# Kernel optimization log

Measured on AMD Instinct MI355X. Metric: run time of the kernel, lower is better.

Reference implementation:

```python
import jax, jax.numpy as jnp
import numpy as np

HIDDEN = 1024
HEADS = 16
HEAD_DIM = HIDDEN // HEADS  # 64
B, S = 2, 2048


def setup_inputs() -> dict:
    key = jax.random.key(0)
    ks = jax.random.split(key, 8)
    scale = 1.0 / np.sqrt(HIDDEN)
    return {
        "hidden_states": jax.random.normal(ks[0], (B, S, HIDDEN), dtype=jnp.float32),
        "head_mask": jnp.ones((1, HEADS, 1, 1), dtype=jnp.float32),
        "Wq": jax.random.normal(ks[1], (HIDDEN, HIDDEN), dtype=jnp.float32) * scale,
        "bq": jnp.zeros((HIDDEN,), dtype=jnp.float32),
        "Wk": jax.random.normal(ks[2], (HIDDEN, HIDDEN), dtype=jnp.float32) * scale,
        "bk": jnp.zeros((HIDDEN,), dtype=jnp.float32),
        "Wv": jax.random.normal(ks[3], (HIDDEN, HIDDEN), dtype=jnp.float32) * scale,
        "bv": jnp.zeros((HIDDEN,), dtype=jnp.float32),
    }


def _split_heads(x):
    # [B, S, HIDDEN] -> [B, HEADS, S, HEAD_DIM]
    b, s, _ = x.shape
    return x.reshape(b, s, HEADS, HEAD_DIM).transpose(0, 2, 1, 3)


def reference(hidden_states, head_mask, Wq, bq, Wk, bk, Wv, bv):
    q = _split_heads(hidden_states @ Wq + bq)
    k = _split_heads(hidden_states @ Wk + bk)
    v = _split_heads(hidden_states @ Wv + bv)
    # [B, H, S, S] attention scores (eager, full matrix as in original)
    scores = jnp.einsum("bhqd,bhkd->bhqk", q, k) / jnp.sqrt(jnp.float32(HEAD_DIM))
    probs = jax.nn.softmax(scores, axis=-1)
    probs = probs * head_mask  # post-softmax multiplicative head mask
    ctx = jnp.einsum("bhqk,bhkd->bhqd", probs, v)
    b, h, s, d = ctx.shape
    return ctx.transpose(0, 2, 1, 3).reshape(b, s, h * d)
```

## Files before the change

kernel.cpp:

```cpp
#include <hip/hip_runtime.h>
#include <hip/hip_bf16.h>
#include <stdint.h>

#define B_  2
#define S_  2048
#define H_  16
#define D_  64
#define HID 1024

typedef __bf16 bf16x8 __attribute__((ext_vector_type(8)));
typedef float  f32x4  __attribute__((ext_vector_type(4)));
typedef float  f32x16 __attribute__((ext_vector_type(16)));
typedef unsigned int u32x4 __attribute__((ext_vector_type(4)));
typedef unsigned short ush;

__device__ __forceinline__ ush f2bf(float f) {
    __bf16 b = (__bf16)f;
    return __builtin_bit_cast(ush, b);
}
__device__ __forceinline__ unsigned pk2(float a, float b) {
    return (unsigned)f2bf(a) | ((unsigned)f2bf(b) << 16);
}
__device__ __forceinline__ float xchg32f(float x) {
    return __shfl_xor(x, 32, 64);
}
__device__ __forceinline__ float exp2fast(float x) {
#if __has_builtin(__builtin_amdgcn_exp2f)
    return __builtin_amdgcn_exp2f(x);
#else
    float r; asm("v_exp_f32 %0, %1" : "=v"(r) : "v"(x)); return r;
#endif
}
__device__ __forceinline__ void gld16(const void* g, void* l) {
    __builtin_amdgcn_global_load_lds(
        (const __attribute__((address_space(1))) unsigned*)g,
        (__attribute__((address_space(3))) unsigned*)l, 16, 0, 0);
}
#define MFMA32(a, b, c) __builtin_amdgcn_mfma_f32_32x32x16_bf16(a, b, c, 0, 0, 0)

__global__ __launch_bounds__(256) void cvt_hid(const float* __restrict__ in,
                                               ush* __restrict__ outp) {
    size_t base = ((size_t)blockIdx.x * 256 + threadIdx.x) * 16;
    #pragma unroll
    for (int half = 0; half < 2; ++half) {
        float4 v0 = *reinterpret_cast<const float4*>(in + base + half * 8);
        float4 v1 = *reinterpret_cast<const float4*>(in + base + half * 8 + 4);
        u32x4 o = { pk2(v0.x, v0.y), pk2(v0.z, v0.w),
                    pk2(v1.x, v1.y), pk2(v1.z, v1.w) };
        *reinterpret_cast<u32x4*>(outp + base + half * 8) = o;
    }
}

__global__ __launch_bounds__(256) void wtrans(
    const float* __restrict__ Wq, const float* __restrict__ Wk,
    const float* __restrict__ Wv, ush* __restrict__ wt)
{
    const int tid = threadIdx.x;
    const int k0 = blockIdx.x * 64, n0 = blockIdx.y * 64, sel = blockIdx.z;
    const float* W = sel == 0 ? Wq : (sel == 1 ? Wk : Wv);
    ush* o = wt + (size_t)sel * HID * HID;
    __shared__ ush lT[64][72];
    #pragma unroll
    for (int i = 0; i < 4; ++i) {
        int c = tid + i * 256;
        int kr = c >> 4, c4 = (c & 15) << 2;
        float4 v = *reinterpret_cast<const float4*>(W + (size_t)(k0 + kr) * HID + n0 + c4);
        lT[kr][c4 + 0] = f2bf(v.x); lT[kr][c4 + 1] = f2bf(v.y);
        lT[kr][c4 + 2] = f2bf(v.z); lT[kr][c4 + 3] = f2bf(v.w);
    }
    __syncthreads();
    #pragma unroll
    for (int i = 0; i < 2; ++i) {
        int c = tid + i * 256;
        int nr = c >> 3, k8 = (c & 7) << 3;
        ush t[8];
        #pragma unroll
        for (int u = 0; u < 8; ++u) t[u] = lT[k8 + u][nr];
        u32x4 ov = { (unsigned)t[0] | ((unsigned)t[1] << 16),
                     (unsigned)t[2] | ((unsigned)t[3] << 16),
                     (unsigned)t[4] | ((unsigned)t[5] << 16),
                     (unsigned)t[6] | ((unsigned)t[7] << 16) };
        *reinterpret_cast<u32x4*>(o + (size_t)(n0 + nr) * HID + k0 + k8) = ov;
    }
}

__global__ __launch_bounds__(256) void proj(
    const ush* __restrict__ hidb, const ush* __restrict__ wt,
    const float* __restrict__ bq, const float* __restrict__ bk,
    const float* __restrict__ bv,
    ush* __restrict__ qd, ush* __restrict__ kd, ush* __restrict__ vtd)
{
    const int tid = threadIdx.x;
    const int wave = tid >> 6, lane = tid & 63;
    const int fr = lane & 15, fq = lane >> 4;
    const int wr = wave >> 1, wc = wave & 1;
    const int m0 = blockIdx.x * 128;
    const int n0 = blockIdx.y * 128;
    const int wsel = n0 >> 10;

    __shared__ char pool[65536];

    const int cr = lane >> 3;
    const int cs = lane & 7;

    f32x4 acc[4][4] = {};

    const ush* Asrc = hidb + (size_t)m0 * HID;
    const ush* Bsrc = wt + (size_t)n0 * HID;

    auto stage = [&](int buf, int kk) {
        #pragma unroll
        for (int j = 0; j < 4; ++j) {
            int ch = wave * 4 + j;
            int r = ch * 8 + cr;
            int so = kk + ((cs ^ (r & 7)) << 3);
            gld16(Asrc + (size_t)r * HID + so, pool + buf * 16384 + ch * 1024);
            gld16(Bsrc + (size_t)r * HID + so, pool + 32768 + buf * 16384 + ch * 1024);
        }
    };

    stage(0, 0);
    __syncthreads();
    int buf = 0;
    for (int ks = 0; ks < 16; ++ks) {
        if (ks < 15) stage(buf ^ 1, (ks + 1) * 64);
        const char* ab = pool + buf * 16384;
        const char* bb = pool + 32768 + buf * 16384;
        #pragma unroll
        for (int c = 0; c < 2; ++c) {
            bf16x8 a[4], b[4];
            #pragma unroll
            for (int i = 0; i < 4; ++i) {
                int ra = wr * 64 + i * 16 + fr;
                a[i] = *reinterpret_cast<const bf16x8*>(
                    ab + ((ra * 128 + c * 64 + fq * 16) ^ ((ra & 7) << 4)));
                int rb = wc * 64 + i * 16 + fr;
                b[i] = *reinterpret_cast<const bf16x8*>(
                    bb + ((rb * 128 + c * 64 + fq * 16) ^ ((rb & 7) << 4)));
            }
            __builtin_amdgcn_s_setprio(1);
            #pragma unroll
            for (int i = 0; i < 4; ++i)
                #pragma unroll
                for (int j = 0; j < 4; ++j)
                    acc[i][j] = __builtin_amdgcn_mfma_f32_16x16x32_bf16(
                        a[i], b[j], acc[i][j], 0, 0, 0);
            __builtin_amdgcn_s_setprio(0);
        }
        __syncthreads();
        buf ^= 1;
    }

    const int bi = m0 >> 11;
    const int s0 = m0 & 2047;
    const float* bias = wsel == 0 ? bq : (wsel == 1 ? bk : bv);
    const int nb = n0 & 1023;

    if (wsel < 2) {
        ush* dst = wsel == 0 ? qd : kd;
        const float scale = wsel == 0 ? 0.18033688011112042f : 1.0f;
        #pragma unroll
        for (int j = 0; j < 4; ++j) {
            int n = nb + wc * 64 + j * 16 + fr;
            int hh = n >> 6, d = n & 63;
            float bb2 = bias[n];
            const size_t rowb = (size_t)(bi * H_ + hh) * S_;
            #pragma unroll
            for (int i = 0; i < 4; ++i)
                #pragma unroll
                for (int e = 0; e < 4; ++e) {
                    int s = s0 + wr * 64 + i * 16 + fq * 4 + e;
                    dst[(rowb + s) * D_ + d] = f2bf((acc[i][j][e] + bb2) * scale);
                }
        }
    } else {
        ush (*lT)[136] = (ush (*)[136])pool;
        #pragma unroll
        for (int j = 0; j < 4; ++j) {
            int nl = wc * 64 + j * 16 + fr;
            float bb2 = bias[nb + nl];
            #pragma unroll
            for (int i = 0; i < 4; ++i)
                #pragma unroll
                for (int e = 0; e < 4; ++e)
                    lT[wr * 64 + i * 16 + fq * 4 + e][nl] = f2bf(acc[i][j][e] + bb2);
        }
        __syncthreads();
        #pragma unroll
        for (int c2 = 0; c2 < 8; ++c2) {
            int cid = tid + c2 * 256;
            int nl = cid >> 4, s8 = (cid & 15) * 8;
            int n = nb + nl, hh = n >> 6, d = n & 63;
            ush t[8];
            #pragma unroll
            for (int u = 0; u < 8; ++u) t[u] = lT[s8 + u][nl];
            u32x4 ov = { (unsigned)t[0] | ((unsigned)t[1] << 16),
                         (unsigned)t[2] | ((unsigned)t[3] << 16),
                         (unsigned)t[4] | ((unsigned)t[5] << 16),
                         (unsigned)t[6] | ((unsigned)t[7] << 16) };
            *reinterpret_cast<u32x4*>(
                vtd + ((size_t)(bi * H_ + hh) * D_ + d) * S_ + s0 + s8) = ov;
        }
    }
}

#define STAGE(sb, kv0) do {                                                    \
    gld16(K + (size_t)((kv0) + kr) * D_ + ss,      pool + (sb) * 16384 + wave * 1024); \
    gld16(K + (size_t)((kv0) + 64 + kr) * D_ + ss, pool + (sb) * 16384 + 8192 + wave * 1024); \
    gld16(VT + (size_t)dr * S_ + (kv0) + ss,       pool + 32768 + (sb) * 16384 + wave * 1024); \
    gld16(VT + (size_t)dr * S_ + (kv0) + 64 + ss,  pool + 32768 + (sb) * 16384 + 8192 + wave * 1024); \
} while (0)

#define WAITV0() asm volatile("s_waitcnt vmcnt(0)" ::: "memory")
#define BARRIER() do { __builtin_amdgcn_s_barrier();                           \
                       __builtin_amdgcn_sched_barrier(0); } while (0)

#define EXPC(cA, cB, pA, pB, hb) do {                                          \
    float a0_ = exp2fast(pA[(hb)+0]), a1_ = exp2fast(pA[(hb)+1]);              \
    float a2_ = exp2fast(pA[(hb)+2]), a3_ = exp2fast(pA[(hb)+3]);              \
    float a4_ = exp2fast(pA[(hb)+4]), a5_ = exp2fast(pA[(hb)+5]);              \
    float a6_ = exp2fast(pA[(hb)+6]), a7_ = exp2fast(pA[(hb)+7]);              \
    sA += ((a0_+a1_)+(a2_+a3_)) + ((a4_+a5_)+(a6_+a7_));                       \
    cA = u32x4{pk2(a0_,a1_), pk2(a2_,a3_), pk2(a4_,a5_), pk2(a6_,a7_)};        \
    float b0_ = exp2fast(pB[(hb)+0]), b1_ = exp2fast(pB[(hb)+1]);              \
    float b2_ = exp2fast(pB[(hb)+2]), b3_ = exp2fast(pB[(hb)+3]);              \
    float b4_ = exp2fast(pB[(hb)+4]), b5_ = exp2fast(pB[(hb)+5]);              \
    float b6_ = exp2fast(pB[(hb)+6]), b7_ = exp2fast(pB[(hb)+7]);              \
    sB += ((b0_+b1_)+(b2_+b3_)) + ((b4_+b5_)+(b6_+b7_));                       \
    cB = u32x4{pk2(b0_,b1_), pk2(b2_,b3_), pk2(b4_,b5_), pk2(b6_,b7_)};        \
} while (0)

#define PVC(ksc, cA, cB) do {                                                  \
    const int o_ = l31 * 128 + (ksc) * 32 + hi * 16;                           \
    bf16x8 v0_ = *(const bf16x8*)(vb + (o_ ^ swz));                            \
    bf16x8 v1_ = *(const bf16x8*)(vb + ((o_ + 4096) ^ swz));                   \
    bf16x8 fA_ = __builtin_bit_cast(bf16x8, cA);                               \
    bf16x8 fB_ = __builtin_bit_cast(bf16x8, cB);                               \
    __builtin_amdgcn_s_setprio(1);                                             \
    aA0 = MFMA32(v0_, fA_, aA0); aA1 = MFMA32(v1_, fA_, aA1);                  \
    aB0 = MFMA32(v0_, fB_, aB0); aB1 = MFMA32(v1_, fB_, aB1);                  \
    __builtin_amdgcn_s_setprio(0);                                             \
} while (0)

__global__ __launch_bounds__(512) void attn(
    const ush* __restrict__ qg, const ush* __restrict__ kg,
    const ush* __restrict__ vtg, const float* __restrict__ hm,
    float* __restrict__ out)
{
    const int tid = threadIdx.x;
    const int wave = tid >> 6, lane = tid & 63;
    const int l31 = lane & 31, hi = lane >> 5;
    const int swz = (l31 & 7) << 4;
    const int g = blockIdx.x & 31, qt = blockIdx.x >> 5;
    const int h = g >> 1, bi = g & 1;
    const int qsub = wave & 3, par = wave >> 2;
    const size_t ho = (size_t)(bi * H_ + h) * S_ * D_;
    const ush* Q  = qg + ho;
    const ush* K  = kg + ho;
    const ush* VT = vtg + ho;

    __shared__ __align__(16) char pool[67584];

    const int dr = wave * 8 + (lane >> 3);
    const int kr = (dr & ~12) | ((dr & 4) << 1) | ((dr & 8) >> 1);
    const int ss = ((lane & 7) ^ (lane >> 3)) * 8;

    const int q0 = qt * 256 + qsub * 64 + l31;
    bf16x8 qfA[4], qfB[4];
    #pragma unroll
    for (int ks = 0; ks < 4; ++ks) {
        qfA[ks] = *reinterpret_cast<const bf16x8*>(Q + (size_t)q0 * D_ + ks * 16 + hi * 8);
        qfB[ks] = *reinterpret_cast<const bf16x8*>(Q + (size_t)(q0 + 32) * D_ + ks * 16 + hi * 8);
    }

    f32x16 aA0 = {}, aA1 = {}, aB0 = {}, aB1 = {};
    float sA = 0.f, sB = 0.f;

    STAGE(0, 0);
    WAITV0(); BARRIER();

    for (int s = 0; s < 16; ++s) {
        if (s < 15) STAGE((s + 1) & 1, (s + 1) * 128);
        const char* kb = pool + (s & 1) * 16384 + par * 8192;
        const char* vb = pool + 32768 + (s & 1) * 16384 + par * 8192;

        f32x16 p0A = {}, p1A = {}, p0B = {}, p1B = {};
        #pragma unroll
        for (int ks = 0; ks < 4; ++ks) {
            const int o = l31 * 128 + ks * 32 + hi * 16;
            bf16x8 k0 = *reinterpret_cast<const bf16x8*>(kb + (o ^ swz));
            bf16x8 k1 = *reinterpret_cast<const bf16x8*>(kb + ((o + 4096) ^ swz));
            __builtin_amdgcn_s_setprio(1);
            p0A = MFMA32(k0, qfA[ks], p0A);
            p1A = MFMA32(k1, qfA[ks], p1A);
            p0B = MFMA32(k0, qfB[ks], p0B);
            p1B = MFMA32(k1, qfB[ks], p1B);
            __builtin_amdgcn_s_setprio(0);
        }

        {
            u32x4 cA0, cB0, cA1, cB1, cA2, cB2, cA3, cB3;
            EXPC(cA0, cB0, p0A, p0B, 0);
            PVC(0, cA0, cB0);
            EXPC(cA1, cB1, p0A, p0B, 8);
            PVC(1, cA1, cB1);
            EXPC(cA2, cB2, p1A, p1B, 0);
            PVC(2, cA2, cB2);
            EXPC(cA3, cB3, p1A, p1B, 8);
            PVC(3, cA3, cB3);
        }

        WAITV0(); BARRIER();
    }

    sA += xchg32f(sA);
    sB += xchg32f(sB);
    float* cbase = (float*)pool;
    float* lbase = (float*)(pool + 65536);

    if (par == 1) {
        #pragma unroll
        for (int c = 0; c < 4; ++c) {
            *(f32x4*)(cbase + qsub * 4096 + (0 * 4 + c) * 256 + lane * 4) =
                f32x4{aA0[c * 4], aA0[c * 4 + 1], aA0[c * 4 + 2], aA0[c * 4 + 3]};
            *(f32x4*)(cbase + qsub * 4096 + (1 * 4 + c) * 256 + lane * 4) =
                f32x4{aA1[c * 4], aA1[c * 4 + 1], aA1[c * 4 + 2], aA1[c * 4 + 3]};
            *(f32x4*)(cbase + qsub * 4096 + (2 * 4 + c) * 256 + lane * 4) =
                f32x4{aB0[c * 4], aB0[c * 4 + 1], aB0[c * 4 + 2], aB0[c * 4 + 3]};
            *(f32x4*)(cbase + qsub * 4096 + (3 * 4 + c) * 256 + lane * 4) =
                f32x4{aB1[c * 4], aB1[c * 4 + 1], aB1[c * 4 + 2], aB1[c * 4 + 3]};
        }
        lbase[qsub * 128 + lane * 2]     = sA;
        lbase[qsub * 128 + lane * 2 + 1] = sB;
    }
    __syncthreads();
    if (par == 0) {
        #pragma unroll
        for (int c = 0; c < 4; ++c) {
            f32x4 t;
            t = *(const f32x4*)(cbase + qsub * 4096 + (0 * 4 + c) * 256 + lane * 4);
            aA0[c*4] += t[0]; aA0[c*4+1] += t[1]; aA0[c*4+2] += t[2]; aA0[c*4+3] += t[3];
            t = *(const f32x4*)(cbase + qsub * 4096 + (1 * 4 + c) * 256 + lane * 4);
            aA1[c*4] += t[0]; aA1[c*4+1] += t[1]; aA1[c*4+2] += t[2]; aA1[c*4+3] += t[3];
            t = *(const f32x4*)(cbase + qsub * 4096 + (2 * 4 + c) * 256 + lane * 4);
            aB0[c*4] += t[0]; aB0[c*4+1] += t[1]; aB0[c*4+2] += t[2]; aB0[c*4+3] += t[3];
            t = *(const f32x4*)(cbase + qsub * 4096 + (3 * 4 + c) * 256 + lane * 4);
            aB1[c*4] += t[0]; aB1[c*4+1] += t[1]; aB1[c*4+2] += t[2]; aB1[c*4+3] += t[3];
        }
        const float liA = sA + lbase[qsub * 128 + lane * 2];
        const float liB = sB + lbase[qsub * 128 + lane * 2 + 1];
        const float hmv = hm[h];
        const float invA = hmv / liA, invB = hmv / liB;
        float* orA = out + ((size_t)bi * S_ + q0) * HID + h * D_;
        float* orB = out + ((size_t)bi * S_ + q0 + 32) * HID + h * D_;
        #pragma unroll
        for (int gg = 0; gg < 4; ++gg) {
            f32x4 o0, o1, o2, o3;
            #pragma unroll
            for (int e = 0; e < 4; ++e) {
                o0[e] = aA0[gg * 4 + e] * invA;
                o1[e] = aA1[gg * 4 + e] * invA;
                o2[e] = aB0[gg * 4 + e] * invB;
                o3[e] = aB1[gg * 4 + e] * invB;
            }
            *reinterpret_cast<f32x4*>(orA + gg * 8 + hi * 4)      = o0;
            *reinterpret_cast<f32x4*>(orA + 32 + gg * 8 + hi * 4) = o1;
            *reinterpret_cast<f32x4*>(orB + gg * 8 + hi * 4)      = o2;
            *reinterpret_cast<f32x4*>(orB + 32 + gg * 8 + hi * 4) = o3;
        }
    }
}

extern "C" void kernel_launch(void* const* d_in, const int* in_sizes, int n_in,
                              void* d_out, int out_size, void* d_ws, size_t ws_size,
                              hipStream_t stream) {
    const float* hid = (const float*)d_in[0];
    const float* hm  = (const float*)d_in[1];
    const float* Wq  = (const float*)d_in[2];
    const float* bq  = (const float*)d_in[3];
    const float* Wk  = (const float*)d_in[4];
    const float* bk  = (const float*)d_in[5];
    const float* Wv  = (const float*)d_in[6];
    const float* bv  = (const float*)d_in[7];
    float* out = (float*)d_out;

    const size_t NE = (size_t)B_ * H_ * S_ * D_;
    ush* qws  = (ush*)d_ws;
    ush* kws  = qws + NE;
    ush* vt   = kws + NE;
    ush* hidb = (ush*)d_out;
    ush* wt   = hidb + NE;

    cvt_hid<<<1024, 256, 0, stream>>>(hid, hidb);
    wtrans<<<dim3(16, 16, 3), 256, 0, stream>>>(Wq, Wk, Wv, wt);
    proj<<<dim3(32, 24), 256, 0, stream>>>(hidb, wt, bq, bk, bv, qws, kws, vt);
    attn<<<256, 512, 0, stream>>>(qws, kws, vt, hm, out);
}
```

Baseline: 89.29 us.

## Load K and V fragments directly from global into registers, dropping LDS staging

```diff
diff --git a/kernel.cpp b/kernel.cpp
--- a/kernel.cpp
+++ b/kernel.cpp
@@ -204,17 +204,6 @@
     }
 }
 
-#define STAGE(sb, kv0) do {                                                    \
-    gld16(K + (size_t)((kv0) + kr) * D_ + ss,      pool + (sb) * 16384 + wave * 1024); \
-    gld16(K + (size_t)((kv0) + 64 + kr) * D_ + ss, pool + (sb) * 16384 + 8192 + wave * 1024); \
-    gld16(VT + (size_t)dr * S_ + (kv0) + ss,       pool + 32768 + (sb) * 16384 + wave * 1024); \
-    gld16(VT + (size_t)dr * S_ + (kv0) + 64 + ss,  pool + 32768 + (sb) * 16384 + 8192 + wave * 1024); \
-} while (0)
-
-#define WAITV0() asm volatile("s_waitcnt vmcnt(0)" ::: "memory")
-#define BARRIER() do { __builtin_amdgcn_s_barrier();                           \
-                       __builtin_amdgcn_sched_barrier(0); } while (0)
-
 #define EXPC(cA, cB, pA, pB, hb) do {                                          \
     float a0_ = exp2fast(pA[(hb)+0]), a1_ = exp2fast(pA[(hb)+1]);              \
     float a2_ = exp2fast(pA[(hb)+2]), a3_ = exp2fast(pA[(hb)+3]);              \
@@ -231,14 +220,11 @@
 } while (0)
 
 #define PVC(ksc, cA, cB) do {                                                  \
-    const int o_ = l31 * 128 + (ksc) * 32 + hi * 16;                           \
-    bf16x8 v0_ = *(const bf16x8*)(vb + (o_ ^ swz));                            \
-    bf16x8 v1_ = *(const bf16x8*)(vb + ((o_ + 4096) ^ swz));                   \
     bf16x8 fA_ = __builtin_bit_cast(bf16x8, cA);                               \
     bf16x8 fB_ = __builtin_bit_cast(bf16x8, cB);                               \
     __builtin_amdgcn_s_setprio(1);                                             \
-    aA0 = MFMA32(v0_, fA_, aA0); aA1 = MFMA32(v1_, fA_, aA1);                  \
-    aB0 = MFMA32(v0_, fB_, aB0); aB1 = MFMA32(v1_, fB_, aB1);                  \
+    aA0 = MFMA32(vfA[ksc], fA_, aA0); aA1 = MFMA32(vfB[ksc], fA_, aA1);        \
+    aB0 = MFMA32(vfA[ksc], fB_, aB0); aB1 = MFMA32(vfB[ksc], fB_, aB1);        \
     __builtin_amdgcn_s_setprio(0);                                             \
 } while (0)
 
@@ -250,7 +236,6 @@
     const int tid = threadIdx.x;
     const int wave = tid >> 6, lane = tid & 63;
     const int l31 = lane & 31, hi = lane >> 5;
-    const int swz = (l31 & 7) << 4;
     const int g = blockIdx.x & 31, qt = blockIdx.x >> 5;
     const int h = g >> 1, bi = g & 1;
     const int qsub = wave & 3, par = wave >> 2;
@@ -261,9 +246,7 @@
 
     __shared__ __align__(16) char pool[67584];
 
-    const int dr = wave * 8 + (lane >> 3);
-    const int kr = (dr & ~12) | ((dr & 4) << 1) | ((dr & 8) >> 1);
-    const int ss = ((lane & 7) ^ (lane >> 3)) * 8;
+    const int krow = (l31 & ~12) | ((l31 & 4) << 1) | ((l31 & 8) >> 1);
 
     const int q0 = qt * 256 + qsub * 64 + l31;
     bf16x8 qfA[4], qfB[4];
@@ -276,26 +259,40 @@
     f32x16 aA0 = {}, aA1 = {}, aB0 = {}, aB1 = {};
     float sA = 0.f, sB = 0.f;
 
-    STAGE(0, 0);
-    WAITV0(); BARRIER();
+    bf16x8 kfA[4], kfB[4], vfA[4], vfB[4];
+
+    int kvw = par * 64;
+    {
+        const ush* kb0 = K + (size_t)(kvw + krow) * D_ + hi * 8;
+        const ush* vb0 = VT + (size_t)l31 * S_ + kvw + hi * 8;
+        #pragma unroll
+        for (int ks = 0; ks < 4; ++ks) {
+            kfA[ks] = *(const bf16x8*)(kb0 + ks * 16);
+            kfB[ks] = *(const bf16x8*)(kb0 + 32 * D_ + ks * 16);
+            vfA[ks] = *(const bf16x8*)(vb0 + ks * 16);
+            vfB[ks] = *(const bf16x8*)(vb0 + 32 * S_ + ks * 16);
+        }
+    }
 
     for (int s = 0; s < 16; ++s) {
-        if (s < 15) STAGE((s + 1) & 1, (s + 1) * 128);
-        const char* kb = pool + (s & 1) * 16384 + par * 8192;
-        const char* vb = pool + 32768 + (s & 1) * 16384 + par * 8192;
-
         f32x16 p0A = {}, p1A = {}, p0B = {}, p1B = {};
+        __builtin_amdgcn_s_setprio(1);
         #pragma unroll
         for (int ks = 0; ks < 4; ++ks) {
-            const int o = l31 * 128 + ks * 32 + hi * 16;
-            bf16x8 k0 = *reinterpret_cast<const bf16x8*>(kb + (o ^ swz));
-            bf16x8 k1 = *reinterpret_cast<const bf16x8*>(kb + ((o + 4096) ^ swz));
-            __builtin_amdgcn_s_setprio(1);
-            p0A = MFMA32(k0, qfA[ks], p0A);
-            p1A = MFMA32(k1, qfA[ks], p1A);
-            p0B = MFMA32(k0, qfB[ks], p0B);
-            p1B = MFMA32(k1, qfB[ks], p1B);
-            __builtin_amdgcn_s_setprio(0);
+            p0A = MFMA32(kfA[ks], qfA[ks], p0A);
+            p1A = MFMA32(kfB[ks], qfA[ks], p1A);
+            p0B = MFMA32(kfA[ks], qfB[ks], p0B);
+            p1B = MFMA32(kfB[ks], qfB[ks], p1B);
+        }
+        __builtin_amdgcn_s_setprio(0);
+
+        if (s < 15) {
+            const ush* kb0 = K + (size_t)(kvw + 128 + krow) * D_ + hi * 8;
+            #pragma unroll
+            for (int ks = 0; ks < 4; ++ks) {
+                kfA[ks] = *(const bf16x8*)(kb0 + ks * 16);
+                kfB[ks] = *(const bf16x8*)(kb0 + 32 * D_ + ks * 16);
+            }
         }
 
         {
@@ -310,7 +307,15 @@
             PVC(3, cA3, cB3);
         }
 
-        WAITV0(); BARRIER();
+        if (s < 15) {
+            const ush* vb0 = VT + (size_t)l31 * S_ + kvw + 128 + hi * 8;
+            #pragma unroll
+            for (int ks = 0; ks < 4; ++ks) {
+                vfA[ks] = *(const bf16x8*)(vb0 + ks * 16);
+                vfB[ks] = *(const bf16x8*)(vb0 + 32 * S_ + ks * 16);
+            }
+        }
+        kvw += 128;
     }
 
     sA += xchg32f(sA);
```

New measurement: 111.3 us. 24.7% more time.

## Split attention KV range four ways per block and double grid size

Applied to the files above, without the earlier changes.

```diff
diff --git a/kernel.cpp b/kernel.cpp
--- a/kernel.cpp
+++ b/kernel.cpp
@@ -205,10 +205,12 @@
 }
 
 #define STAGE(sb, kv0) do {                                                    \
-    gld16(K + (size_t)((kv0) + kr) * D_ + ss,      pool + (sb) * 16384 + wave * 1024); \
-    gld16(K + (size_t)((kv0) + 64 + kr) * D_ + ss, pool + (sb) * 16384 + 8192 + wave * 1024); \
-    gld16(VT + (size_t)dr * S_ + (kv0) + ss,       pool + 32768 + (sb) * 16384 + wave * 1024); \
-    gld16(VT + (size_t)dr * S_ + (kv0) + 64 + ss,  pool + 32768 + (sb) * 16384 + 8192 + wave * 1024); \
+    char* Kb_ = pool + (sb) * 32768;                                           \
+    char* Vb_ = Kb_ + 16384;                                                   \
+    gld16(K + (size_t)((kv0) + kr) * D_ + ss,      Kb_ + wave * 1024);         \
+    gld16(K + (size_t)((kv0) + 64 + kr) * D_ + ss, Kb_ + 8192 + wave * 1024);  \
+    gld16(VT + (size_t)dr * S_ + (kv0) + ss,       Vb_ + wave * 1024);         \
+    gld16(VT + (size_t)dr * S_ + (kv0) + 64 + ss,  Vb_ + 8192 + wave * 1024);  \
 } while (0)
 
 #define WAITV0() asm volatile("s_waitcnt vmcnt(0)" ::: "memory")
@@ -230,8 +232,8 @@
     cB = u32x4{pk2(b0_,b1_), pk2(b2_,b3_), pk2(b4_,b5_), pk2(b6_,b7_)};        \
 } while (0)
 
-#define PVC(ksc, cA, cB) do {                                                  \
-    const int o_ = l31 * 128 + (ksc) * 32 + hi * 16;                           \
+#define PVC(kc, cA, cB) do {                                                   \
+    const int o_ = l31 * 128 + vcol + (kc) * 32 + hi * 16;                     \
     bf16x8 v0_ = *(const bf16x8*)(vb + (o_ ^ swz));                            \
     bf16x8 v1_ = *(const bf16x8*)(vb + ((o_ + 4096) ^ swz));                   \
     bf16x8 fA_ = __builtin_bit_cast(bf16x8, cA);                               \
@@ -240,6 +242,39 @@
     aA0 = MFMA32(v0_, fA_, aA0); aA1 = MFMA32(v1_, fA_, aA1);                  \
     aB0 = MFMA32(v0_, fB_, aB0); aB1 = MFMA32(v1_, fB_, aB1);                  \
     __builtin_amdgcn_s_setprio(0);                                             \
+} while (0)
+
+#define DUMPACC(slot) do {                                                     \
+    _Pragma("unroll")                                                          \
+    for (int c = 0; c < 4; ++c) {                                              \
+        *(f32x4*)(cbase + (slot) * 4096 + (0 * 4 + c) * 256 + lane * 4) =      \
+            f32x4{aA0[c*4], aA0[c*4+1], aA0[c*4+2], aA0[c*4+3]};               \
+        *(f32x4*)(cbase + (slot) * 4096 + (1 * 4 + c) * 256 + lane * 4) =      \
+            f32x4{aA1[c*4], aA1[c*4+1], aA1[c*4+2], aA1[c*4+3]};               \
+        *(f32x4*)(cbase + (slot) * 4096 + (2 * 4 + c) * 256 + lane * 4) =      \
+            f32x4{aB0[c*4], aB0[c*4+1], aB0[c*4+2], aB0[c*4+3]};               \
+        *(f32x4*)(cbase + (slot) * 4096 + (3 * 4 + c) * 256 + lane * 4) =      \
+            f32x4{aB1[c*4], aB1[c*4+1], aB1[c*4+2], aB1[c*4+3]};               \
+    }                                                                          \
+    lbase[(slot) * 128 + lane * 2]     = sA;                                   \
+    lbase[(slot) * 128 + lane * 2 + 1] = sB;                                   \
+} while (0)
+
+#define ADDACC(slot) do {                                                      \
+    _Pragma("unroll")                                                          \
+    for (int c = 0; c < 4; ++c) {                                              \
+        f32x4 t;                                                               \
+        t = *(const f32x4*)(cbase + (slot) * 4096 + (0*4+c) * 256 + lane * 4); \
+        aA0[c*4] += t[0]; aA0[c*4+1] += t[1]; aA0[c*4+2] += t[2]; aA0[c*4+3] += t[3]; \
+        t = *(const f32x4*)(cbase + (slot) * 4096 + (1*4+c) * 256 + lane * 4); \
+        aA1[c*4] += t[0]; aA1[c*4+1] += t[1]; aA1[c*4+2] += t[2]; aA1[c*4+3] += t[3]; \
+        t = *(const f32x4*)(cbase + (slot) * 4096 + (2*4+c) * 256 + lane * 4); \
+        aB0[c*4] += t[0]; aB0[c*4+1] += t[1]; aB0[c*4+2] += t[2]; aB0[c*4+3] += t[3]; \
+        t = *(const f32x4*)(cbase + (slot) * 4096 + (3*4+c) * 256 + lane * 4); \
+        aB1[c*4] += t[0]; aB1[c*4+1] += t[1]; aB1[c*4+2] += t[2]; aB1[c*4+3] += t[3]; \
+    }                                                                          \
+    sA += lbase[(slot) * 128 + lane * 2];                                      \
+    sB += lbase[(slot) * 128 + lane * 2 + 1];                                  \
 } while (0)
 
 __global__ __launch_bounds__(512) void attn(
@@ -253,7 +288,7 @@
     const int swz = (l31 & 7) << 4;
     const int g = blockIdx.x & 31, qt = blockIdx.x >> 5;
     const int h = g >> 1, bi = g & 1;
-    const int qsub = wave & 3, par = wave >> 2;
+    const int qsub = wave & 1, par = wave >> 1;
     const size_t ho = (size_t)(bi * H_ + h) * S_ * D_;
     const ush* Q  = qg + ho;
     const ush* K  = kg + ho;
@@ -265,7 +300,7 @@
     const int kr = (dr & ~12) | ((dr & 4) << 1) | ((dr & 8) >> 1);
     const int ss = ((lane & 7) ^ (lane >> 3)) * 8;
 
-    const int q0 = qt * 256 + qsub * 64 + l31;
+    const int q0 = qt * 128 + qsub * 64 + l31;
     bf16x8 qfA[4], qfB[4];
     #pragma unroll
     for (int ks = 0; ks < 4; ++ks) {
@@ -279,35 +314,29 @@
     STAGE(0, 0);
     WAITV0(); BARRIER();
 
+    const int vcol = (par & 1) * 64;
     for (int s = 0; s < 16; ++s) {
         if (s < 15) STAGE((s + 1) & 1, (s + 1) * 128);
-        const char* kb = pool + (s & 1) * 16384 + par * 8192;
-        const char* vb = pool + 32768 + (s & 1) * 16384 + par * 8192;
-
-        f32x16 p0A = {}, p1A = {}, p0B = {}, p1B = {};
+        const char* kb = pool + (s & 1) * 32768 + (par >> 1) * 8192 + (par & 1) * 4096;
+        const char* vb = pool + (s & 1) * 32768 + 16384 + (par >> 1) * 8192;
+
+        f32x16 p0A = {}, p0B = {};
         #pragma unroll
         for (int ks = 0; ks < 4; ++ks) {
             const int o = l31 * 128 + ks * 32 + hi * 16;
             bf16x8 k0 = *reinterpret_cast<const bf16x8*>(kb + (o ^ swz));
-            bf16x8 k1 = *reinterpret_cast<const bf16x8*>(kb + ((o + 4096) ^ swz));
             __builtin_amdgcn_s_setprio(1);
             p0A = MFMA32(k0, qfA[ks], p0A);
-            p1A = MFMA32(k1, qfA[ks], p1A);
             p0B = MFMA32(k0, qfB[ks], p0B);
-            p1B = MFMA32(k1, qfB[ks], p1B);
             __builtin_amdgcn_s_setprio(0);
         }
 
         {
-            u32x4 cA0, cB0, cA1, cB1, cA2, cB2, cA3, cB3;
+            u32x4 cA0, cB0, cA1, cB1;
             EXPC(cA0, cB0, p0A, p0B, 0);
             PVC(0, cA0, cB0);
             EXPC(cA1, cB1, p0A, p0B, 8);
             PVC(1, cA1, cB1);
-            EXPC(cA2, cB2, p1A, p1B, 0);
-            PVC(2, cA2, cB2);
-            EXPC(cA3, cB3, p1A, p1B, 8);
-            PVC(3, cA3, cB3);
         }
 
         WAITV0(); BARRIER();
@@ -318,39 +347,16 @@
     float* cbase = (float*)pool;
     float* lbase = (float*)(pool + 65536);
 
-    if (par == 1) {
-        #pragma unroll
-        for (int c = 0; c < 4; ++c) {
-            *(f32x4*)(cbase + qsub * 4096 + (0 * 4 + c) * 256 + lane * 4) =
-                f32x4{aA0[c * 4], aA0[c * 4 + 1], aA0[c * 4 + 2], aA0[c * 4 + 3]};
-            *(f32x4*)(cbase + qsub * 4096 + (1 * 4 + c) * 256 + lane * 4) =
-                f32x4{aA1[c * 4], aA1[c * 4 + 1], aA1[c * 4 + 2], aA1[c * 4 + 3]};
-            *(f32x4*)(cbase + qsub * 4096 + (2 * 4 + c) * 256 + lane * 4) =
-                f32x4{aB0[c * 4], aB0[c * 4 + 1], aB0[c * 4 + 2], aB0[c * 4 + 3]};
-            *(f32x4*)(cbase + qsub * 4096 + (3 * 4 + c) * 256 + lane * 4) =
-                f32x4{aB1[c * 4], aB1[c * 4 + 1], aB1[c * 4 + 2], aB1[c * 4 + 3]};
-        }
-        lbase[qsub * 128 + lane * 2]     = sA;
-        lbase[qsub * 128 + lane * 2 + 1] = sB;
-    }
+    if (par >= 2) DUMPACC((par - 2) * 2 + qsub);
+    __syncthreads();
+    if (par < 2) ADDACC(par * 2 + qsub);
+    __syncthreads();
+    if (par == 1) DUMPACC(qsub);
     __syncthreads();
     if (par == 0) {
-        #pragma unroll
-        for (int c = 0; c < 4; ++c) {
-            f32x4 t;
-            t = *(const f32x4*)(cbase + qsub * 4096 + (0 * 4 + c) * 256 + lane * 4);
-            aA0[c*4] += t[0]; aA0[c*4+1] += t[1]; aA0[c*4+2] += t[2]; aA0[c*4+3] += t[3];
-            t = *(const f32x4*)(cbase + qsub * 4096 + (1 * 4 + c) * 256 + lane * 4);
-            aA1[c*4] += t[0]; aA1[c*4+1] += t[1]; aA1[c*4+2] += t[2]; aA1[c*4+3] += t[3];
-            t = *(const f32x4*)(cbase + qsub * 4096 + (2 * 4 + c) * 256 + lane * 4);
-            aB0[c*4] += t[0]; aB0[c*4+1] += t[1]; aB0[c*4+2] += t[2]; aB0[c*4+3] += t[3];
-            t = *(const f32x4*)(cbase + qsub * 4096 + (3 * 4 + c) * 256 + lane * 4);
-            aB1[c*4] += t[0]; aB1[c*4+1] += t[1]; aB1[c*4+2] += t[2]; aB1[c*4+3] += t[3];
-        }
-        const float liA = sA + lbase[qsub * 128 + lane * 2];
-        const float liB = sB + lbase[qsub * 128 + lane * 2 + 1];
+        ADDACC(qsub);
         const float hmv = hm[h];
-        const float invA = hmv / liA, invB = hmv / liB;
+        const float invA = hmv / sA, invB = hmv / sB;
         float* orA = out + ((size_t)bi * S_ + q0) * HID + h * D_;
         float* orB = out + ((size_t)bi * S_ + q0 + 32) * HID + h * D_;
         #pragma unroll
@@ -394,5 +400,5 @@
     cvt_hid<<<1024, 256, 0, stream>>>(hid, hidb);
     wtrans<<<dim3(16, 16, 3), 256, 0, stream>>>(Wq, Wk, Wv, wt);
     proj<<<dim3(32, 24), 256, 0, stream>>>(hidb, wt, bq, bk, bv, qws, kws, vt);
-    attn<<<256, 512, 0, stream>>>(qws, kws, vt, hm, out);
-}
+    attn<<<512, 512, 0, stream>>>(qws, kws, vt, hm, out);
+}
```

Result: slower. 94.18 us (+5.5%).

## Triple-buffer K/V tiles in LDS with two-deep prefetch and full unroll

Applied to the files above, without the earlier changes.

```diff
diff --git a/kernel.cpp b/kernel.cpp
--- a/kernel.cpp
+++ b/kernel.cpp
@@ -205,12 +205,13 @@
 }
 
 #define STAGE(sb, kv0) do {                                                    \
-    gld16(K + (size_t)((kv0) + kr) * D_ + ss,      pool + (sb) * 16384 + wave * 1024); \
-    gld16(K + (size_t)((kv0) + 64 + kr) * D_ + ss, pool + (sb) * 16384 + 8192 + wave * 1024); \
-    gld16(VT + (size_t)dr * S_ + (kv0) + ss,       pool + 32768 + (sb) * 16384 + wave * 1024); \
-    gld16(VT + (size_t)dr * S_ + (kv0) + 64 + ss,  pool + 32768 + (sb) * 16384 + 8192 + wave * 1024); \
+    gld16(K + (size_t)((kv0) + kr) * D_ + ss,      pool + (sb) * 32768 + wave * 1024); \
+    gld16(K + (size_t)((kv0) + 64 + kr) * D_ + ss, pool + (sb) * 32768 + 8192 + wave * 1024); \
+    gld16(VT + (size_t)dr * S_ + (kv0) + ss,       pool + (sb) * 32768 + 16384 + wave * 1024); \
+    gld16(VT + (size_t)dr * S_ + (kv0) + 64 + ss,  pool + (sb) * 32768 + 24576 + wave * 1024); \
 } while (0)
 
+#define WAITV4() asm volatile("s_waitcnt vmcnt(4)" ::: "memory")
 #define WAITV0() asm volatile("s_waitcnt vmcnt(0)" ::: "memory")
 #define BARRIER() do { __builtin_amdgcn_s_barrier();                           \
                        __builtin_amdgcn_sched_barrier(0); } while (0)
@@ -240,6 +241,41 @@
     aA0 = MFMA32(v0_, fA_, aA0); aA1 = MFMA32(v1_, fA_, aA1);                  \
     aB0 = MFMA32(v0_, fB_, aB0); aB1 = MFMA32(v1_, fB_, aB1);                  \
     __builtin_amdgcn_s_setprio(0);                                             \
+} while (0)
+
+#define COMP(bc) do {                                                          \
+    const char* kb = pool + (bc) * 32768 + par * 8192;                         \
+    const char* vb = pool + (bc) * 32768 + 16384 + par * 8192;                 \
+    f32x16 p0A = {}, p1A = {}, p0B = {}, p1B = {};                             \
+    _Pragma("unroll")                                                          \
+    for (int ks = 0; ks < 4; ++ks) {                                           \
+        const int o = l31 * 128 + ks * 32 + hi * 16;                           \
+        bf16x8 k0 = *reinterpret_cast<const bf16x8*>(kb + (o ^ swz));          \
+        bf16x8 k1 = *reinterpret_cast<const bf16x8*>(kb + ((o + 4096) ^ swz)); \
+        __builtin_amdgcn_s_setprio(1);                                         \
+        p0A = MFMA32(k0, qfA[ks], p0A);                                        \
+        p1A = MFMA32(k1, qfA[ks], p1A);                                        \
+        p0B = MFMA32(k0, qfB[ks], p0B);                                        \
+        p1B = MFMA32(k1, qfB[ks], p1B);                                        \
+        __builtin_amdgcn_s_setprio(0);                                         \
+    }                                                                          \
+    {                                                                          \
+        u32x4 cA0, cB0, cA1, cB1, cA2, cB2, cA3, cB3;                          \
+        EXPC(cA0, cB0, p0A, p0B, 0);                                           \
+        PVC(0, cA0, cB0);                                                      \
+        EXPC(cA1, cB1, p0A, p0B, 8);                                           \
+        PVC(1, cA1, cB1);                                                      \
+        EXPC(cA2, cB2, p1A, p1B, 0);                                           \
+        PVC(2, cA2, cB2);                                                      \
+        EXPC(cA3, cB3, p1A, p1B, 8);                                           \
+        PVC(3, cA3, cB3);                                                      \
+    }                                                                          \
+} while (0)
+
+#define FSTEP(t) do {                                                          \
+    STAGE(((t) + 2) % 3, ((t) + 2) * 128);                                     \
+    COMP((t) % 3);                                                             \
+    WAITV4(); BARRIER();                                                       \
 } while (0)
 
 __global__ __launch_bounds__(512) void attn(
@@ -259,7 +295,7 @@
     const ush* K  = kg + ho;
     const ush* VT = vtg + ho;
 
-    __shared__ __align__(16) char pool[67584];
+    __shared__ __align__(16) char pool[100352];
 
     const int dr = wave * 8 + (lane >> 3);
     const int kr = (dr & ~12) | ((dr & 4) << 1) | ((dr & 8) >> 1);
@@ -277,46 +313,22 @@
     float sA = 0.f, sB = 0.f;
 
     STAGE(0, 0);
+    STAGE(1, 128);
+    WAITV4(); BARRIER();
+
+    FSTEP(0);  FSTEP(1);  FSTEP(2);  FSTEP(3);
+    FSTEP(4);  FSTEP(5);  FSTEP(6);  FSTEP(7);
+    FSTEP(8);  FSTEP(9);  FSTEP(10); FSTEP(11);
+    FSTEP(12); FSTEP(13);
+    COMP(14 % 3);
     WAITV0(); BARRIER();
-
-    for (int s = 0; s < 16; ++s) {
-        if (s < 15) STAGE((s + 1) & 1, (s + 1) * 128);
-        const char* kb = pool + (s & 1) * 16384 + par * 8192;
-        const char* vb = pool + 32768 + (s & 1) * 16384 + par * 8192;
-
-        f32x16 p0A = {}, p1A = {}, p0B = {}, p1B = {};
-        #pragma unroll
-        for (int ks = 0; ks < 4; ++ks) {
-            const int o = l31 * 128 + ks * 32 + hi * 16;
-            bf16x8 k0 = *reinterpret_cast<const bf16x8*>(kb + (o ^ swz));
-            bf16x8 k1 = *reinterpret_cast<const bf16x8*>(kb + ((o + 4096) ^ swz));
-            __builtin_amdgcn_s_setprio(1);
-            p0A = MFMA32(k0, qfA[ks], p0A);
-            p1A = MFMA32(k1, qfA[ks], p1A);
-            p0B = MFMA32(k0, qfB[ks], p0B);
-            p1B = MFMA32(k1, qfB[ks], p1B);
-            __builtin_amdgcn_s_setprio(0);
-        }
-
-        {
-            u32x4 cA0, cB0, cA1, cB1, cA2, cB2, cA3, cB3;
-            EXPC(cA0, cB0, p0A, p0B, 0);
-            PVC(0, cA0, cB0);
-            EXPC(cA1, cB1, p0A, p0B, 8);
-            PVC(1, cA1, cB1);
-            EXPC(cA2, cB2, p1A, p1B, 0);
-            PVC(2, cA2, cB2);
-            EXPC(cA3, cB3, p1A, p1B, 8);
-            PVC(3, cA3, cB3);
-        }
-
-        WAITV0(); BARRIER();
-    }
+    COMP(15 % 3);
+    __syncthreads();
 
     sA += xchg32f(sA);
     sB += xchg32f(sB);
     float* cbase = (float*)pool;
-    float* lbase = (float*)(pool + 65536);
+    float* lbase = (float*)(pool + 98304);
 
     if (par == 1) {
         #pragma unroll
```

New measurement: 172.2 us. +92.9%, slower.
